# Kernel tuning notes

Measured on AMD Instinct MI355X. Metric: run time of the kernel, lower is better.

Reference implementation:

```python
import jax, jax.numpy as jnp
import numpy as np

TOPK, NUM_CLASSES = 13, 80
ALPHA, BETA, GAMMA, EPS = 1.0, 5.0, 3.0, 1e-09


def _make_boxes(key, shape, img=640.0, wmin=10.0, wmax=120.0):
    k1, k2 = jax.random.split(key)
    cxy = jax.random.uniform(k1, shape[:-1] + (2,), minval=0.0, maxval=img)
    wh = jax.random.uniform(k2, shape[:-1] + (2,), minval=wmin, maxval=wmax)
    return jnp.concatenate([cxy - wh / 2, cxy + wh / 2], axis=-1)


def setup_inputs() -> dict:
    key = jax.random.key(0)
    ks = jax.random.split(key, 7)
    bs, A, C, n = 16, 8400, 80, 60
    return {
        'pd_scores': jax.random.uniform(ks[0], (bs, A, C), dtype=jnp.float32),
        'pd_bboxes': _make_boxes(ks[1], (bs, A, 4)),
        'pd_angles': jax.random.uniform(ks[2], (bs, A, 1), minval=0.0, maxval=90.0),
        'anc_points': jax.random.uniform(ks[3], (A, 2), minval=0.0, maxval=640.0),
        'gt_labels': jax.random.randint(ks[4], (bs, n, 1), 0, C, dtype=jnp.int32),
        'gt_bboxes': _make_boxes(ks[5], (bs, n, 4)),
        'gt_angles': jax.random.uniform(ks[6], (bs, n, 1), minval=0.0, maxval=90.0),
        'mask_gt': jnp.ones((bs, n, 1), jnp.float32),
        'epoch_num': 1,
    }


def _cos_fn(x, ar, beta=2.0):
    return 0.5 + 0.5 * jnp.cos(beta / ar * x / 180.0 * jnp.pi + jnp.pi * (1.0 - beta / (2.0 * ar)))


def _angle_measure(pd_angles, gt_angles, gt_bboxes):
    # gt area ratio w/h -> (bs, n, 1, 1)
    w = gt_bboxes[..., 2:3] - gt_bboxes[..., 0:1]
    h = gt_bboxes[..., 3:4] - gt_bboxes[..., 1:2]
    ar = (w / (h + 1e-05))[:, :, None, :]
    theta = jnp.abs(gt_angles[:, :, None, :] - pd_angles[:, None, :, :])  # (bs,n,A,1)
    av = 1.0 / ar / (2.0 - 1.0 / ar)
    mx = _cos_fn(0.0, ar)
    mn = _cos_fn(90.0, ar)
    r = (_cos_fn(theta, ar) - mn) / (mx - mn) * (1.0 - av) + av
    r = jnp.where(jnp.isnan(r), 0.0, r)
    return jnp.squeeze(r, -1)  # (bs, n, A)


def _pairwise_iou(gt, pd):
    # gt (bs,n,4), pd (bs,A,4) -> (bs,n,A)
    lt = jnp.maximum(gt[:, :, None, :2], pd[:, None, :, :2])
    rb = jnp.minimum(gt[:, :, None, 2:], pd[:, None, :, 2:])
    inter = jnp.clip(rb - lt, 0.0).prod(-1)
    a1 = jnp.clip(gt[..., 2:] - gt[..., :2], 0.0).prod(-1)[:, :, None]
    a2 = jnp.clip(pd[..., 2:] - pd[..., :2], 0.0).prod(-1)[:, None, :]
    return inter / (a1 + a2 - inter + EPS)


def _select_topk(metrics, topk_mask):
    bs, n, A = metrics.shape
    _, idxs = jax.lax.top_k(metrics, TOPK)
    idxs = jnp.where(topk_mask, idxs, 0)
    flat = idxs.reshape(bs * n, TOPK)
    cnt = jnp.zeros((bs * n, A), jnp.int32).at[jnp.arange(bs * n)[:, None], flat].add(1)
    cnt = cnt.reshape(bs, n, A)
    return jnp.where(cnt > 1, 0, cnt).astype(metrics.dtype)


def _select_highest_overlaps(mask_pos, overlaps, n):
    fg = mask_pos.sum(-2)                                   # (bs, A)
    multi = fg[:, None, :] > 1                              # (bs, 1, A)
    is_max = jax.nn.one_hot(overlaps.argmax(1), n, axis=1, dtype=mask_pos.dtype)  # (bs,n,A)
    mask_pos = jnp.where(multi, is_max, mask_pos)
    fg = mask_pos.sum(-2)
    tgt_idx = mask_pos.argmax(-2)                           # (bs, A)
    return tgt_idx, fg, mask_pos


def reference(pd_scores, pd_bboxes, pd_angles, anc_points, gt_labels, gt_bboxes, gt_angles, mask_gt, epoch_num):
    bs, A, C = pd_scores.shape
    n = gt_bboxes.shape[1]
    lab = gt_labels[..., 0].astype(jnp.int32)               # (bs, n)

    # bbox_scores: pd_scores[b, :, gt_label] -> (bs, n, A)
    pts = jnp.transpose(pd_scores, (0, 2, 1))               # (bs, C, A)
    bbox_scores = jnp.take_along_axis(pts, lab[:, :, None], axis=1)

    overlaps = _pairwise_iou(gt_bboxes, pd_bboxes)          # (bs, n, A)
    ang = _angle_measure(pd_angles, gt_angles, gt_bboxes)   # (bs, n, A)
    align = bbox_scores ** ALPHA * overlaps ** BETA * ang ** GAMMA

    # anchors-inside-gt mask (bs, n, A)
    lt = anc_points[None, None, :, :] - gt_bboxes[:, :, None, :2]
    rb = gt_bboxes[:, :, None, 2:] - anc_points[None, None, :, :]
    in_gts = (jnp.concatenate([lt, rb], -1).min(-1) > EPS).astype(align.dtype)

    topk_mask = jnp.broadcast_to(mask_gt > 0, (bs, n, TOPK))
    mask_topk = _select_topk(align * in_gts, topk_mask)
    mask_pos = mask_topk * in_gts * mask_gt                 # (bs, n, A)

    tgt_idx, fg, mask_pos = _select_highest_overlaps(mask_pos, overlaps, n)

    # gather per-anchor targets from flattened gt tensors
    off = tgt_idx + jnp.arange(bs, dtype=tgt_idx.dtype)[:, None] * n   # (bs, A)
    tlab = lab.reshape(-1)[off]
    tlab = jnp.where(tlab < 0, 0, tlab)
    tbb = gt_bboxes.reshape(-1, 4)[off]                     # (bs, A, 4)
    tang = gt_angles.reshape(-1, 1)[off]                    # (bs, A, 1)
    ts = jax.nn.one_hot(tlab, C, dtype=pd_scores.dtype)     # (bs, A, C)
    ts = jnp.where(fg[:, :, None] > 0, ts, 0.0)

    # normalized alignment metric scaling
    align = align * mask_pos
    pam = align.max(-1, keepdims=True)                      # (bs, n, 1)
    pov = (overlaps * mask_pos).max(-1, keepdims=True)      # (bs, n, 1)
    norm = (align * pov / (pam + EPS)).max(-2)[:, :, None]  # (bs, A, 1)
    ts = ts * norm

    return tlab, tbb, tang, ts, fg > 0
```

## Files before the change

### kernel.cpp

```cpp
#include <hip/hip_runtime.h>
#include <math.h>

#define TOPK 13
#define PI_F 3.14159265358979323846f

typedef unsigned int u32;
typedef unsigned long long u64;

__device__ __forceinline__ u32 ford(float f) {
    u32 u = __float_as_uint(f);
    return (u & 0x80000000u) ? ~u : (u | 0x80000000u);
}
__device__ __forceinline__ float funord(u32 o) {
    u32 u = (o & 0x80000000u) ? (o & 0x7FFFFFFFu) : ~o;
    return __uint_as_float(u);
}

__device__ __forceinline__ float iou_fn(float4 g, float4 p) {
    float ltx = fmaxf(g.x, p.x), lty = fmaxf(g.y, p.y);
    float rbx = fminf(g.z, p.z), rby = fminf(g.w, p.w);
    float inter = fmaxf(rbx - ltx, 0.0f) * fmaxf(rby - lty, 0.0f);
    float a1 = fmaxf(g.z - g.x, 0.0f) * fmaxf(g.w - g.y, 0.0f);
    float a2 = fmaxf(p.z - p.x, 0.0f) * fmaxf(p.w - p.y, 0.0f);
    return inter / (((a1 + a2) - inter) + 1e-9f);
}

struct RowParams { float av, bar, offc, mx, mn; };

__device__ __forceinline__ RowParams row_params(float4 g) {
    float w = g.z - g.x, h = g.w - g.y;
    float ar = w / (h + 1e-5f);
    float ia = 1.0f / ar;
    RowParams rp;
    rp.av = ia / (2.0f - ia);
    rp.bar = 2.0f / ar;
    rp.offc = PI_F * (1.0f - 2.0f / (2.0f * ar));
    rp.mx = 0.5f + 0.5f * cosf(rp.offc);
    rp.mn = 0.5f + 0.5f * cosf(rp.bar * 90.0f / 180.0f * PI_F + rp.offc);
    return rp;
}

__device__ __forceinline__ float ang_measure(const RowParams& rp, float theta) {
    float cfv = 0.5f + 0.5f * cosf(rp.bar * theta / 180.0f * PI_F + rp.offc);
    float r = (cfv - rp.mn) / (rp.mx - rp.mn) * (1.0f - rp.av) + rp.av;
    return isnan(r) ? 0.0f : r;
}

__device__ __forceinline__ float align_fn(float s, float iou, float r) {
    float iou2 = iou * iou;
    float iou5 = (iou2 * iou2) * iou;
    float r3 = (r * r) * r;
    return (s * iou5) * r3;
}

__global__ void k0_init(int* cnt, int* assign1, u32* pam, u32* pov, int BA, int BN) {
    int t = blockIdx.x * blockDim.x + threadIdx.x;
    if (t < BA) { cnt[t] = 0; assign1[t] = -1; }
    if (t < BN) { pam[t] = 0x80000000u; pov[t] = 0x80000000u; }
}

__global__ __launch_bounds__(256)
void k1_topk(const float* __restrict__ scores, const float* __restrict__ pbox,
             const float* __restrict__ pang, const float* __restrict__ anc,
             const int* __restrict__ glab, const float* __restrict__ gbox,
             const float* __restrict__ gang, const float* __restrict__ mgt,
             int* __restrict__ cnt, int* __restrict__ assign1,
             int bs, int A, int n, int C) {
    int j = blockIdx.x;
    int b = j % bs;
    int i = j / bs;
    int bi = b * n + i;
    int tid = threadIdx.x;

    float mg = mgt[bi];
    if (!(mg > 0.0f)) return;

    float4 g = ((const float4*)gbox)[bi];
    int lab = glab[bi];
    float ga = gang[bi];
    RowParams rp = row_params(g);

    const float4* pb = ((const float4*)pbox) + (size_t)b * A;
    const float* pa = pang + (size_t)b * A;
    const float2* ac = (const float2*)anc;
    const float* sc = scores + (size_t)b * A * C + lab;

    u64 arr[TOPK];
#pragma unroll
    for (int jj = 0; jj < TOPK; jj++) arr[jj] = 0ull;
    u64 zkey = 0ull;

    for (int a = tid; a < A; a += 256) {
        float4 p = pb[a];
        float iou = iou_fn(g, p);
        float2 apt = ac[a];
        float mnv = fminf(fminf(apt.x - g.x, apt.y - g.y), fminf(g.z - apt.x, g.w - apt.y));
        bool inGt = mnv > 1e-9f;
        float th = fabsf(ga - pa[a]);
        float r = ang_measure(rp, th);

        bool zeroCand;
        if (inGt && iou > 0.0f && r > 0.0f) {
            float s = sc[(size_t)a * C];
            float v = align_fn(s, iou, r);
            if (v > 0.0f) {
                zeroCand = false;
                u64 key = ((u64)ford(v) << 32) | (u64)(0xFFFFFFFFu - (u32)a);
                if (key > arr[TOPK - 1]) {
#pragma unroll
                    for (int jj = 0; jj < TOPK; jj++) {
                        u64 hi = arr[jj] > key ? arr[jj] : key;
                        u64 lo = arr[jj] > key ? key : arr[jj];
                        arr[jj] = hi;
                        key = lo;
                    }
                }
            } else {
                zeroCand = true;
            }
        } else {
            zeroCand = (r >= 0.0f);
        }
        if (zeroCand && zkey == 0ull) {
            zkey = (0x80000000ull << 32) | (u64)(0xFFFFFFFFu - (u32)a);
        }
    }
    if (zkey > arr[TOPK - 1]) {
        u64 key = zkey;
#pragma unroll
        for (int jj = 0; jj < TOPK; jj++) {
            u64 hi = arr[jj] > key ? arr[jj] : key;
            u64 lo = arr[jj] > key ? key : arr[jj];
            arr[jj] = hi;
            key = lo;
        }
    }

    __shared__ u64 sh[2][4];
    int lane = tid & 63, wv = tid >> 6;
    for (int round = 0; round < TOPK; round++) {
        u64 head = arr[0];
        u64 m = head;
#pragma unroll
        for (int st = 32; st > 0; st >>= 1) {
            u64 o = __shfl_xor(m, st, 64);
            if (o > m) m = o;
        }
        if (lane == 0) sh[round & 1][wv] = m;
        __syncthreads();
        u64 win = sh[round & 1][0];
        u64 w1 = sh[round & 1][1]; if (w1 > win) win = w1;
        u64 w2 = sh[round & 1][2]; if (w2 > win) win = w2;
        u64 w3 = sh[round & 1][3]; if (w3 > win) win = w3;
        if (head == win && win != 0ull) {
#pragma unroll
            for (int jj = 0; jj < TOPK - 1; jj++) arr[jj] = arr[jj + 1];
            arr[TOPK - 1] = 0ull;
            int a = (int)(0xFFFFFFFFu - (u32)(win & 0xFFFFFFFFull));
            float2 apt = ac[a];
            float mnv = fminf(fminf(apt.x - g.x, apt.y - g.y), fminf(g.z - apt.x, g.w - apt.y));
            if (mnv > 1e-9f) {
                atomicAdd(&cnt[(size_t)b * A + a], 1);
                atomicMax(&assign1[(size_t)b * A + a], i);
            }
        }
    }
}

__global__ __launch_bounds__(256)
void k2_resolve(const float* __restrict__ scores, const float* __restrict__ pbox,
                const float* __restrict__ pang, const int* __restrict__ glab,
                const float* __restrict__ gbox, const float* __restrict__ gang,
                const int* __restrict__ cnt, const int* __restrict__ assign1,
                int* __restrict__ assign, float* __restrict__ alignv,
                u32* __restrict__ pam, u32* __restrict__ pov,
                int bs, int A, int n, int C) {
    int t = blockIdx.x * blockDim.x + threadIdx.x;
    if (t >= bs * A) return;
    int b = t / A;
    int c = cnt[t];
    int asg = -1;
    float alv = 0.0f;
    if (c > 0) {
        float4 p = ((const float4*)pbox)[t];
        if (c == 1) {
            asg = assign1[t];
        } else {
            float best = -1.0f;
            asg = 0;
            for (int i = 0; i < n; i++) {
                float4 gi = ((const float4*)gbox)[b * n + i];
                float io = iou_fn(gi, p);
                if (io > best) { best = io; asg = i; }
            }
        }
        float4 g = ((const float4*)gbox)[b * n + asg];
        RowParams rp = row_params(g);
        float iou = iou_fn(g, p);
        float th = fabsf(gang[b * n + asg] - pang[t]);
        float r = ang_measure(rp, th);
        float s = scores[(size_t)t * C + glab[b * n + asg]];
        alv = align_fn(s, iou, r);
        atomicMax(&pam[b * n + asg], ford(alv));
        atomicMax(&pov[b * n + asg], ford(iou));
    }
    assign[t] = asg;
    alignv[t] = alv;
}

__global__ __launch_bounds__(256)
void k3_out(const int* __restrict__ glab, const float* __restrict__ gbox,
            const float* __restrict__ gang, const int* __restrict__ assign,
            const float* __restrict__ alignv, const u32* __restrict__ pam,
            const u32* __restrict__ pov, float* __restrict__ out,
            int bs, int A, int n, int C) {
    __shared__ float s_nv[256];
    __shared__ int s_lf[256];
    int tid = threadIdx.x;
    int base = blockIdx.x * 256;
    int t = base + tid;
    int BA = bs * A;

    if (t < BA) {
        int b = t / A;
        int asg = assign[t];
        bool fg = asg >= 0;
        int tgt = fg ? asg : 0;
        int lb = glab[b * n + tgt];
        if (lb < 0) lb = 0;

        float* o_tlab = out;
        float* o_tbb = out + BA;
        float* o_tang = out + (size_t)BA * 5;
        float* o_fg = out + (size_t)BA * 6 + (size_t)BA * C;

        o_tlab[t] = (float)lb;
        ((float4*)o_tbb)[t] = ((const float4*)gbox)[b * n + tgt];
        o_tang[t] = gang[b * n + tgt];
        o_fg[t] = fg ? 1.0f : 0.0f;

        float nv = 0.0f;
        if (fg) {
            float pamv = funord(pam[b * n + asg]);
            float povv = funord(pov[b * n + asg]);
            float vv = (alignv[t] * povv) / (pamv + 1e-9f);
            nv = fmaxf(vv, 0.0f);
        }
        s_nv[tid] = nv;
        s_lf[tid] = fg ? lb : -1;
    } else {
        s_nv[tid] = 0.0f;
        s_lf[tid] = -1;
    }
    __syncthreads();

    int Q = C / 4;
    int nA = min(256, BA - base);
    if (nA <= 0) return;
    int total = nA * Q;
    float4* o_ts = (float4*)(out + (size_t)BA * 6) + (size_t)base * Q;
    for (int idx = tid; idx < total; idx += 256) {
        int tl = idx / Q;
        int q = idx - tl * Q;
        float nv = s_nv[tl];
        int lf = s_lf[tl];
        int cb = q * 4;
        float4 o;
        o.x = (lf == cb) ? nv : 0.0f;
        o.y = (lf == cb + 1) ? nv : 0.0f;
        o.z = (lf == cb + 2) ? nv : 0.0f;
        o.w = (lf == cb + 3) ? nv : 0.0f;
        o_ts[idx] = o;
    }
}

extern "C" void kernel_launch(void* const* d_in, const int* in_sizes, int n_in,
                              void* d_out, int out_size, void* d_ws, size_t ws_size,
                              hipStream_t stream) {
    const float* scores = (const float*)d_in[0];
    const float* pbox = (const float*)d_in[1];
    const float* pang = (const float*)d_in[2];
    const float* anc = (const float*)d_in[3];
    const int* glab = (const int*)d_in[4];
    const float* gbox = (const float*)d_in[5];
    const float* gang = (const float*)d_in[6];
    const float* mgt = (const float*)d_in[7];

    const int C = 80;
    int A = in_sizes[3] / 2;
    int bs = in_sizes[0] / (A * C);
    int n = in_sizes[4] / bs;
    int BA = bs * A;
    int BN = bs * n;

    char* ws = (char*)d_ws;
    int* cnt = (int*)ws;        ws += sizeof(int) * (size_t)BA;
    int* assign1 = (int*)ws;    ws += sizeof(int) * (size_t)BA;
    int* assign = (int*)ws;     ws += sizeof(int) * (size_t)BA;
    float* alignv = (float*)ws; ws += sizeof(float) * (size_t)BA;
    u32* pam = (u32*)ws;        ws += sizeof(u32) * (size_t)BN;
    u32* pov = (u32*)ws;        ws += sizeof(u32) * (size_t)BN;

    k0_init<<<(BA + 255) / 256, 256, 0, stream>>>(cnt, assign1, pam, pov, BA, BN);
    k1_topk<<<BN, 256, 0, stream>>>(scores, pbox, pang, anc, glab, gbox, gang, mgt,
                                    cnt, assign1, bs, A, n, C);
    k2_resolve<<<(BA + 255) / 256, 256, 0, stream>>>(scores, pbox, pang, glab, gbox, gang,
                                                     cnt, assign1, assign, alignv, pam, pov,
                                                     bs, A, n, C);
    k3_out<<<(BA + 255) / 256, 256, 0, stream>>>(glab, gbox, gang, assign, alignv, pam, pov,
                                                 (float*)d_out, bs, A, n, C);
}
```

Baseline: 171.4 us.

## Skip non-candidate anchor work and merge top-k per wave without block barriers

The top-k kernel now checks the in-box test first and only loads the predicted box, computes IoU and angle measures when the anchor can be a candidate or the zero-key fallback is still unset. The cross-wave top-k merge no longer calls __syncthreads once per round. Each wave records its 13 winners in shared memory, and after a single barrier wave 0 merges them. The block also grows to 512 threads. Together these cut wasted loads, transcendental work and synchronisation, at the cost of more divergent branches.

```diff
diff --git a/kernel.cpp b/kernel.cpp
--- a/kernel.cpp
+++ b/kernel.cpp
@@ -3,6 +3,8 @@
 
 #define TOPK 13
 #define PI_F 3.14159265358979323846f
+#define K1_THREADS 512
+#define K1_WAVES (K1_THREADS / 64)
 
 typedef unsigned int u32;
 typedef unsigned long long u64;
@@ -59,7 +61,7 @@
     if (t < BN) { pam[t] = 0x80000000u; pov[t] = 0x80000000u; }
 }
 
-__global__ __launch_bounds__(256)
+__global__ __launch_bounds__(K1_THREADS)
 void k1_topk(const float* __restrict__ scores, const float* __restrict__ pbox,
              const float* __restrict__ pang, const float* __restrict__ anc,
              const int* __restrict__ glab, const float* __restrict__ gbox,
@@ -90,39 +92,45 @@
     for (int jj = 0; jj < TOPK; jj++) arr[jj] = 0ull;
     u64 zkey = 0ull;
 
-    for (int a = tid; a < A; a += 256) {
-        float4 p = pb[a];
-        float iou = iou_fn(g, p);
+    for (int a = tid; a < A; a += K1_THREADS) {
         float2 apt = ac[a];
         float mnv = fminf(fminf(apt.x - g.x, apt.y - g.y), fminf(g.z - apt.x, g.w - apt.y));
         bool inGt = mnv > 1e-9f;
-        float th = fabsf(ga - pa[a]);
-        float r = ang_measure(rp, th);
-
-        bool zeroCand;
-        if (inGt && iou > 0.0f && r > 0.0f) {
-            float s = sc[(size_t)a * C];
-            float v = align_fn(s, iou, r);
-            if (v > 0.0f) {
-                zeroCand = false;
-                u64 key = ((u64)ford(v) << 32) | (u64)(0xFFFFFFFFu - (u32)a);
-                if (key > arr[TOPK - 1]) {
-#pragma unroll
-                    for (int jj = 0; jj < TOPK; jj++) {
-                        u64 hi = arr[jj] > key ? arr[jj] : key;
-                        u64 lo = arr[jj] > key ? key : arr[jj];
-                        arr[jj] = hi;
-                        key = lo;
+        float iou = 0.0f;
+        bool needAlign = false;
+        if (inGt) {
+            float4 p = pb[a];
+            iou = iou_fn(g, p);
+            needAlign = iou > 0.0f;
+        }
+        if (needAlign || zkey == 0ull) {
+            float th = fabsf(ga - pa[a]);
+            float r = ang_measure(rp, th);
+            bool zeroCand;
+            if (needAlign && r > 0.0f) {
+                float s = sc[(size_t)a * C];
+                float v = align_fn(s, iou, r);
+                if (v > 0.0f) {
+                    zeroCand = false;
+                    u64 key = ((u64)ford(v) << 32) | (u64)(0xFFFFFFFFu - (u32)a);
+                    if (key > arr[TOPK - 1]) {
+#pragma unroll
+                        for (int jj = 0; jj < TOPK; jj++) {
+                            u64 hi = arr[jj] > key ? arr[jj] : key;
+                            u64 lo = arr[jj] > key ? key : arr[jj];
+                            arr[jj] = hi;
+                            key = lo;
+                        }
                     }
+                } else {
+                    zeroCand = true;
                 }
             } else {
-                zeroCand = true;
-            }
-        } else {
-            zeroCand = (r >= 0.0f);
-        }
-        if (zeroCand && zkey == 0ull) {
-            zkey = (0x80000000ull << 32) | (u64)(0xFFFFFFFFu - (u32)a);
+                zeroCand = (r >= 0.0f);
+            }
+            if (zeroCand && zkey == 0ull) {
+                zkey = (0x80000000ull << 32) | (u64)(0xFFFFFFFFu - (u32)a);
+            }
         }
     }
     if (zkey > arr[TOPK - 1]) {
@@ -136,32 +144,46 @@
         }
     }
 
-    __shared__ u64 sh[2][4];
+    __shared__ u64 wtop[K1_WAVES * TOPK];
     int lane = tid & 63, wv = tid >> 6;
     for (int round = 0; round < TOPK; round++) {
-        u64 head = arr[0];
-        u64 m = head;
+        u64 m = arr[0];
 #pragma unroll
         for (int st = 32; st > 0; st >>= 1) {
             u64 o = __shfl_xor(m, st, 64);
             if (o > m) m = o;
         }
-        if (lane == 0) sh[round & 1][wv] = m;
-        __syncthreads();
-        u64 win = sh[round & 1][0];
-        u64 w1 = sh[round & 1][1]; if (w1 > win) win = w1;
-        u64 w2 = sh[round & 1][2]; if (w2 > win) win = w2;
-        u64 w3 = sh[round & 1][3]; if (w3 > win) win = w3;
-        if (head == win && win != 0ull) {
+        if (lane == 0) wtop[wv * TOPK + round] = m;
+        if (arr[0] == m && m != 0ull) {
 #pragma unroll
             for (int jj = 0; jj < TOPK - 1; jj++) arr[jj] = arr[jj + 1];
             arr[TOPK - 1] = 0ull;
-            int a = (int)(0xFFFFFFFFu - (u32)(win & 0xFFFFFFFFull));
-            float2 apt = ac[a];
-            float mnv = fminf(fminf(apt.x - g.x, apt.y - g.y), fminf(g.z - apt.x, g.w - apt.y));
-            if (mnv > 1e-9f) {
-                atomicAdd(&cnt[(size_t)b * A + a], 1);
-                atomicMax(&assign1[(size_t)b * A + a], i);
+        }
+    }
+    __syncthreads();
+
+    if (wv == 0) {
+        const int NK = K1_WAVES * TOPK;
+        u64 ka = wtop[lane];
+        u64 kb = (lane + 64 < NK) ? wtop[lane + 64] : 0ull;
+        for (int round = 0; round < TOPK; round++) {
+            u64 m = ka > kb ? ka : kb;
+#pragma unroll
+            for (int st = 32; st > 0; st >>= 1) {
+                u64 o = __shfl_xor(m, st, 64);
+                if (o > m) m = o;
+            }
+            if (m == 0ull) break;
+            if (ka == m || kb == m) {
+                if (ka == m) ka = 0ull; else kb = 0ull;
+                int a = (int)(0xFFFFFFFFu - (u32)(m & 0xFFFFFFFFull));
+                float2 apt = ac[a];
+                float mnv = fminf(fminf(apt.x - g.x, apt.y - g.y),
+                                  fminf(g.z - apt.x, g.w - apt.y));
+                if (mnv > 1e-9f) {
+                    atomicAdd(&cnt[(size_t)b * A + a], 1);
+                    atomicMax(&assign1[(size_t)b * A + a], i);
+                }
             }
         }
     }
@@ -302,8 +324,8 @@
     u32* pov = (u32*)ws;        ws += sizeof(u32) * (size_t)BN;
 
     k0_init<<<(BA + 255) / 256, 256, 0, stream>>>(cnt, assign1, pam, pov, BA, BN);
-    k1_topk<<<BN, 256, 0, stream>>>(scores, pbox, pang, anc, glab, gbox, gang, mgt,
-                                    cnt, assign1, bs, A, n, C);
+    k1_topk<<<BN, K1_THREADS, 0, stream>>>(scores, pbox, pang, anc, glab, gbox, gang, mgt,
+                                           cnt, assign1, bs, A, n, C);
     k2_resolve<<<(BA + 255) / 256, 256, 0, stream>>>(scores, pbox, pang, glab, gbox, gang,
                                                      cnt, assign1, assign, alignv, pam, pov,
                                                      bs, A, n, C);
```

New measurement: 178.0 us. +3.9%, slower.

## Split top-k into anchor-parallel candidate compaction and per-row warp selection

Applied to the files above, without the earlier changes.

Replaces the per-gt row kernel, which scanned all anchors with 256 threads, with two kernels. The first is anchor-parallel: it caches gt row parameters in LDS and appends positive align candidates into a per-row buffer of up to 128 entries using atomics. The second uses one wavefront per gt row to pick the top 13 from that compacted buffer. It finds zero-value fallback candidates with an early-exit ballot scan and falls back to a full scan when the buffer overflows. This avoids a full per-row scan over 8400 anchors and the block-level syncs in each selection round, at the cost of extra atomics, a workspace buffer and an extra launch.

```diff
diff --git a/kernel.cpp b/kernel.cpp
--- a/kernel.cpp
+++ b/kernel.cpp
@@ -3,6 +3,7 @@
 
 #define TOPK 13
 #define PI_F 3.14159265358979323846f
+#define CAP 128
 
 typedef unsigned int u32;
 typedef unsigned long long u64;
@@ -53,80 +54,8 @@
     return (s * iou5) * r3;
 }
 
-__global__ void k0_init(int* cnt, int* assign1, u32* pam, u32* pov, int BA, int BN) {
-    int t = blockIdx.x * blockDim.x + threadIdx.x;
-    if (t < BA) { cnt[t] = 0; assign1[t] = -1; }
-    if (t < BN) { pam[t] = 0x80000000u; pov[t] = 0x80000000u; }
-}
-
-__global__ __launch_bounds__(256)
-void k1_topk(const float* __restrict__ scores, const float* __restrict__ pbox,
-             const float* __restrict__ pang, const float* __restrict__ anc,
-             const int* __restrict__ glab, const float* __restrict__ gbox,
-             const float* __restrict__ gang, const float* __restrict__ mgt,
-             int* __restrict__ cnt, int* __restrict__ assign1,
-             int bs, int A, int n, int C) {
-    int j = blockIdx.x;
-    int b = j % bs;
-    int i = j / bs;
-    int bi = b * n + i;
-    int tid = threadIdx.x;
-
-    float mg = mgt[bi];
-    if (!(mg > 0.0f)) return;
-
-    float4 g = ((const float4*)gbox)[bi];
-    int lab = glab[bi];
-    float ga = gang[bi];
-    RowParams rp = row_params(g);
-
-    const float4* pb = ((const float4*)pbox) + (size_t)b * A;
-    const float* pa = pang + (size_t)b * A;
-    const float2* ac = (const float2*)anc;
-    const float* sc = scores + (size_t)b * A * C + lab;
-
-    u64 arr[TOPK];
-#pragma unroll
-    for (int jj = 0; jj < TOPK; jj++) arr[jj] = 0ull;
-    u64 zkey = 0ull;
-
-    for (int a = tid; a < A; a += 256) {
-        float4 p = pb[a];
-        float iou = iou_fn(g, p);
-        float2 apt = ac[a];
-        float mnv = fminf(fminf(apt.x - g.x, apt.y - g.y), fminf(g.z - apt.x, g.w - apt.y));
-        bool inGt = mnv > 1e-9f;
-        float th = fabsf(ga - pa[a]);
-        float r = ang_measure(rp, th);
-
-        bool zeroCand;
-        if (inGt && iou > 0.0f && r > 0.0f) {
-            float s = sc[(size_t)a * C];
-            float v = align_fn(s, iou, r);
-            if (v > 0.0f) {
-                zeroCand = false;
-                u64 key = ((u64)ford(v) << 32) | (u64)(0xFFFFFFFFu - (u32)a);
-                if (key > arr[TOPK - 1]) {
-#pragma unroll
-                    for (int jj = 0; jj < TOPK; jj++) {
-                        u64 hi = arr[jj] > key ? arr[jj] : key;
-                        u64 lo = arr[jj] > key ? key : arr[jj];
-                        arr[jj] = hi;
-                        key = lo;
-                    }
-                }
-            } else {
-                zeroCand = true;
-            }
-        } else {
-            zeroCand = (r >= 0.0f);
-        }
-        if (zeroCand && zkey == 0ull) {
-            zkey = (0x80000000ull << 32) | (u64)(0xFFFFFFFFu - (u32)a);
-        }
-    }
-    if (zkey > arr[TOPK - 1]) {
-        u64 key = zkey;
+__device__ __forceinline__ void insert13(u64* arr, u64 key) {
+    if (key > arr[TOPK - 1]) {
 #pragma unroll
         for (int jj = 0; jj < TOPK; jj++) {
             u64 hi = arr[jj] > key ? arr[jj] : key;
@@ -135,30 +64,179 @@
             key = lo;
         }
     }
-
-    __shared__ u64 sh[2][4];
-    int lane = tid & 63, wv = tid >> 6;
+}
+
+__global__ void k0_init(int* cnt, int* assign1, u32* pam, u32* pov, int* rowcnt,
+                        int BA, int BN) {
+    int t = blockIdx.x * blockDim.x + threadIdx.x;
+    if (t < BA) { cnt[t] = 0; assign1[t] = -1; }
+    if (t < BN) { pam[t] = 0x80000000u; pov[t] = 0x80000000u; rowcnt[t] = 0; }
+}
+
+__global__ __launch_bounds__(256)
+void k1a_pairs(const float* __restrict__ scores, const float* __restrict__ pbox,
+               const float* __restrict__ pang, const float* __restrict__ anc,
+               const int* __restrict__ glab, const float* __restrict__ gbox,
+               const float* __restrict__ gang, const float* __restrict__ mgt,
+               int* __restrict__ rowcnt, u64* __restrict__ rowbuf,
+               int bs, int A, int n, int C) {
+    extern __shared__ float4 rowdat[];
+    int b = blockIdx.x % bs;
+    int chunk = blockIdx.x / bs;
+    int tid = threadIdx.x;
+
+    for (int i = tid; i < n; i += 256) {
+        int bi = b * n + i;
+        float4 g = ((const float4*)gbox)[bi];
+        RowParams rp = row_params(g);
+        float4 r1 = make_float4(rp.av, rp.bar, rp.offc, gang[bi]);
+        float4 r2 = make_float4(rp.mx, rp.mn, __int_as_float(glab[bi]), mgt[bi]);
+        rowdat[i * 3 + 0] = g;
+        rowdat[i * 3 + 1] = r1;
+        rowdat[i * 3 + 2] = r2;
+    }
+    __syncthreads();
+
+    int a = chunk * 256 + tid;
+    if (a >= A) return;
+
+    float2 apt = ((const float2*)anc)[a];
+    float4 p = ((const float4*)pbox)[(size_t)b * A + a];
+    float pav = pang[(size_t)b * A + a];
+    const float* sc = scores + ((size_t)b * A + a) * C;
+    u32 akey = 0xFFFFFFFFu - (u32)a;
+
+    for (int i = 0; i < n; i++) {
+        float4 r2 = rowdat[i * 3 + 2];
+        if (!(r2.w > 0.0f)) continue;
+        float4 g = rowdat[i * 3 + 0];
+        float mnv = fminf(fminf(apt.x - g.x, apt.y - g.y), fminf(g.z - apt.x, g.w - apt.y));
+        float iou = iou_fn(g, p);
+        if (mnv > 1e-9f && iou > 0.0f) {
+            float4 r1 = rowdat[i * 3 + 1];
+            RowParams rp; rp.av = r1.x; rp.bar = r1.y; rp.offc = r1.z;
+            rp.mx = r2.x; rp.mn = r2.y;
+            float th = fabsf(r1.w - pav);
+            float r = ang_measure(rp, th);
+            if (r > 0.0f) {
+                float s = sc[__float_as_int(r2.z)];
+                float v = align_fn(s, iou, r);
+                if (v > 0.0f) {
+                    int bi = b * n + i;
+                    int pos = atomicAdd(&rowcnt[bi], 1);
+                    if (pos < CAP)
+                        rowbuf[(size_t)bi * CAP + pos] = ((u64)ford(v) << 32) | (u64)akey;
+                }
+            }
+        }
+    }
+}
+
+__global__ __launch_bounds__(64)
+void k1b_select(const float* __restrict__ scores, const float* __restrict__ pbox,
+                const float* __restrict__ pang, const float* __restrict__ anc,
+                const int* __restrict__ glab, const float* __restrict__ gbox,
+                const float* __restrict__ gang, const float* __restrict__ mgt,
+                const int* __restrict__ rowcnt, const u64* __restrict__ rowbuf,
+                int* __restrict__ cnt, int* __restrict__ assign1,
+                int bs, int A, int n, int C) {
+    int bi = blockIdx.x;
+    int b = bi / n, i = bi - b * n;
+    if (!(mgt[bi] > 0.0f)) return;
+    int lane = threadIdx.x;
+
+    float4 g = ((const float4*)gbox)[bi];
+    RowParams rp = row_params(g);
+    float ga = gang[bi];
+    int lab = glab[bi];
+    const float4* pb = (const float4*)pbox + (size_t)b * A;
+    const float* pa = pang + (size_t)b * A;
+    const float2* ac = (const float2*)anc;
+    const float* sc = scores + (size_t)b * A * C + lab;
+
+    __shared__ u64 zlist[16];
+    int found = 0;
+    for (int base = 0; base < A && found < 13; base += 64) {
+        int a = base + lane;
+        bool zc = false;
+        if (a < A) {
+            float2 apt = ac[a];
+            float mnv = fminf(fminf(apt.x - g.x, apt.y - g.y), fminf(g.z - apt.x, g.w - apt.y));
+            float4 p = pb[a];
+            float iou = iou_fn(g, p);
+            float th = fabsf(ga - pa[a]);
+            float r = ang_measure(rp, th);
+            bool na = (mnv > 1e-9f) && (iou > 0.0f);
+            if (na && r > 0.0f) {
+                float s = sc[(size_t)a * C];
+                float v = align_fn(s, iou, r);
+                zc = !(v > 0.0f);
+            } else {
+                zc = (r >= 0.0f);
+            }
+        }
+        u64 bal = __ballot(zc);
+        int below = (int)__popcll(bal & ((1ull << lane) - 1ull));
+        int idx = found + below;
+        if (zc && idx < 13)
+            zlist[idx] = (0x80000000ull << 32) | (u64)(0xFFFFFFFFu - (u32)a);
+        found += (int)__popcll(bal);
+    }
+    __syncthreads();
+    if (found > 13) found = 13;
+
+    u64 arr[TOPK];
+#pragma unroll
+    for (int jj = 0; jj < TOPK; jj++) arr[jj] = 0ull;
+    int pc = rowcnt[bi];
+    if (pc <= CAP) {
+        const u64* buf = rowbuf + (size_t)bi * CAP;
+        u64 ka = (lane < pc) ? buf[lane] : 0ull;
+        u64 kb = (lane + 64 < pc) ? buf[lane + 64] : 0ull;
+        arr[0] = ka > kb ? ka : kb;
+        arr[1] = ka > kb ? kb : ka;
+    } else {
+        for (int a = lane; a < A; a += 64) {
+            float2 apt = ac[a];
+            float mnv = fminf(fminf(apt.x - g.x, apt.y - g.y), fminf(g.z - apt.x, g.w - apt.y));
+            if (!(mnv > 1e-9f)) continue;
+            float4 p = pb[a];
+            float iou = iou_fn(g, p);
+            if (!(iou > 0.0f)) continue;
+            float th = fabsf(ga - pa[a]);
+            float r = ang_measure(rp, th);
+            if (!(r > 0.0f)) continue;
+            float s = sc[(size_t)a * C];
+            float v = align_fn(s, iou, r);
+            if (!(v > 0.0f)) continue;
+            insert13(arr, ((u64)ford(v) << 32) | (u64)(0xFFFFFFFFu - (u32)a));
+        }
+    }
+
+    u64 kz = (lane < found) ? zlist[lane] : 0ull;
     for (int round = 0; round < TOPK; round++) {
-        u64 head = arr[0];
-        u64 m = head;
+        u64 m = arr[0] > kz ? arr[0] : kz;
 #pragma unroll
         for (int st = 32; st > 0; st >>= 1) {
             u64 o = __shfl_xor(m, st, 64);
             if (o > m) m = o;
         }
-        if (lane == 0) sh[round & 1][wv] = m;
-        __syncthreads();
-        u64 win = sh[round & 1][0];
-        u64 w1 = sh[round & 1][1]; if (w1 > win) win = w1;
-        u64 w2 = sh[round & 1][2]; if (w2 > win) win = w2;
-        u64 w3 = sh[round & 1][3]; if (w3 > win) win = w3;
-        if (head == win && win != 0ull) {
+        if (m == 0ull) break;
+        bool own = false;
+        if (arr[0] == m) {
 #pragma unroll
             for (int jj = 0; jj < TOPK - 1; jj++) arr[jj] = arr[jj + 1];
             arr[TOPK - 1] = 0ull;
-            int a = (int)(0xFFFFFFFFu - (u32)(win & 0xFFFFFFFFull));
+            own = true;
+        } else if (kz == m) {
+            kz = 0ull;
+            own = true;
+        }
+        if (own) {
+            int a = (int)(0xFFFFFFFFu - (u32)(m & 0xFFFFFFFFull));
             float2 apt = ac[a];
-            float mnv = fminf(fminf(apt.x - g.x, apt.y - g.y), fminf(g.z - apt.x, g.w - apt.y));
+            float mnv = fminf(fminf(apt.x - g.x, apt.y - g.y),
+                              fminf(g.z - apt.x, g.w - apt.y));
             if (mnv > 1e-9f) {
                 atomicAdd(&cnt[(size_t)b * A + a], 1);
                 atomicMax(&assign1[(size_t)b * A + a], i);
@@ -294,16 +372,23 @@
     int BN = bs * n;
 
     char* ws = (char*)d_ws;
+    u64* rowbuf = (u64*)ws;     ws += sizeof(u64) * (size_t)BN * CAP;
     int* cnt = (int*)ws;        ws += sizeof(int) * (size_t)BA;
     int* assign1 = (int*)ws;    ws += sizeof(int) * (size_t)BA;
     int* assign = (int*)ws;     ws += sizeof(int) * (size_t)BA;
     float* alignv = (float*)ws; ws += sizeof(float) * (size_t)BA;
     u32* pam = (u32*)ws;        ws += sizeof(u32) * (size_t)BN;
     u32* pov = (u32*)ws;        ws += sizeof(u32) * (size_t)BN;
-
-    k0_init<<<(BA + 255) / 256, 256, 0, stream>>>(cnt, assign1, pam, pov, BA, BN);
-    k1_topk<<<BN, 256, 0, stream>>>(scores, pbox, pang, anc, glab, gbox, gang, mgt,
-                                    cnt, assign1, bs, A, n, C);
+    int* rowcnt = (int*)ws;     ws += sizeof(int) * (size_t)BN;
+
+    int nCh = (A + 255) / 256;
+    size_t ldsz = (size_t)n * 3 * sizeof(float4);
+
+    k0_init<<<(BA + 255) / 256, 256, 0, stream>>>(cnt, assign1, pam, pov, rowcnt, BA, BN);
+    k1a_pairs<<<bs * nCh, 256, ldsz, stream>>>(scores, pbox, pang, anc, glab, gbox, gang,
+                                               mgt, rowcnt, rowbuf, bs, A, n, C);
+    k1b_select<<<BN, 64, 0, stream>>>(scores, pbox, pang, anc, glab, gbox, gang, mgt,
+                                      rowcnt, rowbuf, cnt, assign1, bs, A, n, C);
     k2_resolve<<<(BA + 255) / 256, 256, 0, stream>>>(scores, pbox, pang, glab, gbox, gang,
                                                      cnt, assign1, assign, alignv, pam, pov,
                                                      bs, A, n, C);
```

After: 235.6 us. 37.5% more time.
